# Kernel tuning notes

Measured on AMD Instinct MI355X. Metric: run time of the kernel, lower is better.

Reference implementation:

```python
import jax, jax.numpy as jnp
import numpy as np
from jax import lax

DIM = 128
HEADS = 4
HEAD_DIM = DIM // HEADS          # 32
SR = 2
BN_EPS = 1e-5


def setup_inputs() -> dict:
    key = jax.random.key(0)
    ks = jax.random.split(key, 16)
    B, N, C = 8, 3136, DIM
    H = W = 56
    Nkv = (H // SR) * (W // SR)  # 784
    s = 0.05
    inp = {
        "x": jax.random.normal(ks[0], (B, N, C), jnp.float32),
        "relative_pos": jax.random.normal(ks[1], (HEADS, N, Nkv), jnp.float32),
        "Wq": jax.random.normal(ks[2], (C, C), jnp.float32) * s,
        "bq": jnp.zeros((C,), jnp.float32),
        "Wk": jax.random.normal(ks[3], (C, C), jnp.float32) * s,
        "bk": jnp.zeros((C,), jnp.float32),
        "Wv": jax.random.normal(ks[4], (C, C), jnp.float32) * s,
        "bv": jnp.zeros((C,), jnp.float32),
        "conv_w": jax.random.normal(ks[5], (C, 1, SR, SR), jnp.float32) * s,  # depthwise OIHW
        "conv_b": jnp.zeros((C,), jnp.float32),
        "bn_gamma": jnp.ones((C,), jnp.float32),
        "bn_beta": jnp.zeros((C,), jnp.float32),
        "bn_mean": jax.random.normal(ks[6], (C,), jnp.float32) * 0.1,
        "bn_var": jax.random.uniform(ks[7], (C,), jnp.float32, 0.5, 1.5),
        "Wp": jax.random.normal(ks[8], (C, C), jnp.float32) * s,
        "bp": jnp.zeros((C,), jnp.float32),
        "H": H,
        "W": W,
    }
    return inp


def reference(x, relative_pos, Wq, bq, Wk, bk, Wv, bv, conv_w, conv_b,
              bn_gamma, bn_beta, bn_mean, bn_var, Wp, bp, H, W):
    B, N, C = x.shape
    scale = HEAD_DIM ** -0.5

    # q: (B, heads, N, head_dim)
    q = (x @ Wq + bq).reshape(B, N, HEADS, HEAD_DIM).transpose(0, 2, 1, 3)

    # spatial reduction: depthwise conv stride SR + BatchNorm (eval, running stats)
    x_img = x.transpose(0, 2, 1).reshape(B, C, H, W)
    y = lax.conv_general_dilated(
        x_img, conv_w, window_strides=(SR, SR), padding="VALID",
        feature_group_count=C,
        dimension_numbers=("NCHW", "OIHW", "NCHW")) + conv_b[None, :, None, None]
    inv = bn_gamma * lax.rsqrt(bn_var + BN_EPS)
    y = y * inv[None, :, None, None] + (bn_beta - bn_mean * inv)[None, :, None, None]
    x_ = y.reshape(B, C, -1).transpose(0, 2, 1)  # (B, Nkv, C)
    Nkv = x_.shape[1]

    k = (x_ @ Wk + bk).reshape(B, Nkv, HEADS, HEAD_DIM).transpose(0, 2, 1, 3)
    v = (x_ @ Wv + bv).reshape(B, Nkv, HEADS, HEAD_DIM).transpose(0, 2, 1, 3)

    attn = jnp.einsum("bhnd,bhmd->bhnm", q, k) * scale + relative_pos[None]
    attn = jax.nn.softmax(attn, axis=-1)
    out = jnp.einsum("bhnm,bhmd->bhnd", attn, v)
    out = out.transpose(0, 2, 1, 3).reshape(B, N, C)
    return out @ Wp + bp
```

## Files before the change

kernel.cpp:

```cpp
#include <hip/hip_runtime.h>
#include <hip/hip_bf16.h>

#define BATCH 8
#define NQ 3136
#define CDIM 128
#define NHEAD 4
#define HD 32
#define NKV 784
#define HIMG 56
#define SCALE 0.17677669529663687f

typedef __attribute__((ext_vector_type(8))) short bf8_t;
typedef __attribute__((ext_vector_type(4))) float f4_t;

using bf16 = __hip_bfloat16;
using u16  = unsigned short;

static __device__ __forceinline__ float b2f(bf16 v){ return __bfloat162float(v); }
static __device__ __forceinline__ bf16  f2b(float v){ return __float2bfloat16(v); }
static __device__ __forceinline__ short f2s(float v){
  union { bf16 b; short s; } u; u.b = f2b(v); return u.s;
}
static __device__ __forceinline__ float ld1(const void* p, size_t i, int f){
  return f ? b2f(((const bf16*)p)[i]) : ((const float*)p)[i];
}
static __device__ __forceinline__ bf8_t ld8(const void* p, size_t i, int f){
  if (f) return *(const bf8_t*)((const bf16*)p + i);
  const float* fp = (const float*)p + i;
  float4 a = *(const float4*)fp;
  float4 b = *(const float4*)(fp + 4);
  bf8_t r;
  r[0]=f2s(a.x); r[1]=f2s(a.y); r[2]=f2s(a.z); r[3]=f2s(a.w);
  r[4]=f2s(b.x); r[5]=f2s(b.y); r[6]=f2s(b.z); r[7]=f2s(b.w);
  return r;
}
static __device__ __forceinline__ int detect_flag(const void* var_raw){
  const u16* h = (const u16*)var_raw;
  int lane = threadIdx.x & 63;
  bool ok = true;
  #pragma unroll
  for (int t = 0; t < 2; t++){
    union { u16 u; bf16 b; } cv; cv.u = h[lane + 64*t];
    float v = b2f(cv.b);
    ok = ok && (v > 0.3f) && (v < 1.7f);
  }
  return (__ballot(ok) == ~0ull) ? 1 : 0;
}

static __device__ __forceinline__ void mfma_row(
    const bf8_t a[4], const bf16* __restrict__ Wt, int m, int g, f4_t acc[8])
{
  #pragma unroll
  for (int ct = 0; ct < 8; ct++){
    f4_t c = {0.f,0.f,0.f,0.f};
    const bf16* bp = Wt + (size_t)(ct*16 + m)*CDIM + 8*g;
    #pragma unroll
    for (int ks = 0; ks < 4; ks++){
      bf8_t b = *(const bf8_t*)(bp + 32*ks);
      c = __builtin_amdgcn_mfma_f32_16x16x32_bf16(a[ks], b, c, 0,0,0);
    }
    acc[ct] = c;
  }
}

__global__ __launch_bounds__(256) void prep_kernel(
    const void* __restrict__ Wq, const void* __restrict__ Wk,
    const void* __restrict__ Wv, const void* __restrict__ Wp,
    const void* __restrict__ var, const void* __restrict__ cw,
    const void* __restrict__ cb, const void* __restrict__ gam,
    const void* __restrict__ bet, const void* __restrict__ mea,
    const void* __restrict__ bq, const void* __restrict__ bk,
    const void* __restrict__ bv, const void* __restrict__ bp,
    bf16* __restrict__ Wqt, bf16* __restrict__ Wkt,
    bf16* __restrict__ Wvt, bf16* __restrict__ Wpt,
    bf16* __restrict__ bqs, bf16* __restrict__ bks,
    bf16* __restrict__ bvs, bf16* __restrict__ bps,
    float* __restrict__ cwf, float* __restrict__ inv, float* __restrict__ shift2)
{
  int f = detect_flag(var);
  int idx = blockIdx.x*256 + threadIdx.x;
  int mat = idx >> 14;
  int e   = idx & 16383;
  int o = e >> 7, i = e & 127;
  const void* src; bf16* dst; float s = 1.f;
  if      (mat == 0){ src = Wq; dst = Wqt; s = SCALE; }
  else if (mat == 1){ src = Wk; dst = Wkt; }
  else if (mat == 2){ src = Wv; dst = Wvt; }
  else              { src = Wp; dst = Wpt; }
  dst[e] = f2b(ld1(src, (size_t)i*128 + o, f) * s);

  if (blockIdx.x == 0){
    int t = threadIdx.x;
    cwf[t]       = ld1(cw, t, f);
    cwf[t + 256] = ld1(cw, t + 256, f);
    if (t < 128){
      bqs[t] = f2b(ld1(bq, t, f) * SCALE);
      bks[t] = f2b(ld1(bk, t, f));
      bvs[t] = f2b(ld1(bv, t, f));
      bps[t] = f2b(ld1(bp, t, f));
      float iv = ld1(gam, t, f) * rsqrtf(ld1(var, t, f) + 1e-5f);
      inv[t] = iv;
      shift2[t] = ld1(bet, t, f) - ld1(mea, t, f) * iv + ld1(cb, t, f) * iv;
    }
  }
}

__global__ __launch_bounds__(256) void fat_kernel(
    const void* __restrict__ x, const void* __restrict__ var,
    const float* __restrict__ cwf, const float* __restrict__ inv,
    const float* __restrict__ shift2, bf16* __restrict__ xr,
    const bf16* __restrict__ Wqt, const bf16* __restrict__ bqs,
    bf16* __restrict__ qbf)
{
  int f = detect_flag(var);
  if (blockIdx.x < 3136){
    int idx = blockIdx.x*256 + threadIdx.x;
    int c  = idx & 127;
    int t  = idx >> 7;
    int b  = t / NKV;
    int kv = t - b*NKV;
    int i = kv/28, j = kv - i*28;
    size_t base = (size_t)(b*NQ + 2*i*HIMG + 2*j)*CDIM + c;
    float acc = ld1(x, base, f)                   * cwf[c*4 + 0]
              + ld1(x, base + CDIM, f)            * cwf[c*4 + 1]
              + ld1(x, base + HIMG*CDIM, f)       * cwf[c*4 + 2]
              + ld1(x, base + HIMG*CDIM + CDIM, f)* cwf[c*4 + 3];
    xr[idx] = f2b(acc * inv[c] + shift2[c]);
  } else {
    int wave = threadIdx.x >> 6, lane = threadIdx.x & 63;
    int m = lane & 15, g = lane >> 4;
    int task = (blockIdx.x - 3136)*4 + wave;
    int row0 = task*16;
    bf8_t a[4];
    #pragma unroll
    for (int ks = 0; ks < 4; ks++)
      a[ks] = ld8(x, (size_t)(row0 + m)*CDIM + 8*g + 32*ks, f);
    f4_t acc[8];
    mfma_row(a, Wqt, m, g, acc);
    #pragma unroll
    for (int ct = 0; ct < 8; ct++){
      int col = ct*16 + m;
      float bv = b2f(bqs[col]);
      #pragma unroll
      for (int r = 0; r < 4; r++)
        qbf[(size_t)(row0 + 4*g + r)*CDIM + col] = f2b(acc[ct][r] + bv);
    }
  }
}

__global__ __launch_bounds__(256) void kv_kernel(
    const bf16* __restrict__ xr,
    const bf16* __restrict__ Wkt, const bf16* __restrict__ Wvt,
    const bf16* __restrict__ bks, const bf16* __restrict__ bvs,
    bf16* __restrict__ kbf, bf16* __restrict__ vtb)
{
  int wave = threadIdx.x >> 6, lane = threadIdx.x & 63;
  int m = lane & 15, g = lane >> 4;
  bool isK = blockIdx.x < 98;
  int bx = isK ? blockIdx.x : blockIdx.x - 98;
  int row0 = (bx*4 + wave)*16;
  bf8_t a[4];
  #pragma unroll
  for (int ks = 0; ks < 4; ks++)
    a[ks] = *(const bf8_t*)(xr + (size_t)(row0 + m)*CDIM + 8*g + 32*ks);
  f4_t acc[8];
  mfma_row(a, isK ? Wkt : Wvt, m, g, acc);

  if (isK){
    #pragma unroll
    for (int ct = 0; ct < 8; ct++){
      int col = ct*16 + m;
      float bv = b2f(bks[col]);
      #pragma unroll
      for (int r = 0; r < 4; r++)
        kbf[(size_t)(row0 + 4*g + r)*CDIM + col] = f2b(acc[ct][r] + bv);
    }
  } else {
    int b   = row0 / NKV;
    int kv0 = row0 - b*NKV + 4*g;
    #pragma unroll
    for (int ct = 0; ct < 8; ct++){
      int col = ct*16 + m;
      float bv = b2f(bvs[col]);
      int h = col >> 5, d = col & 31;
      union { bf16 hh[4]; uint2 u; } pk;
      #pragma unroll
      for (int r = 0; r < 4; r++) pk.hh[r] = f2b(acc[ct][r] + bv);
      *(uint2*)(vtb + (size_t)((b*NHEAD + h)*HD + d)*NKV + kv0) = pk.u;
    }
  }
}

template<int W>
static __device__ __forceinline__ void stage_rel(
    const void* __restrict__ rel, int f, bf16* __restrict__ rel_l,
    size_t rowbase, int kv0)
{
  const int tid = threadIdx.x;
  if (f){
    constexpr int PER = W/8;
    constexpr int SL  = 64*PER;
    #pragma unroll
    for (int it = 0; it < (SL + 255)/256; it++){
      int s0 = it*256 + tid;
      if (SL < 256 && s0 >= SL) continue;
      int row = s0 / PER;
      int col = (s0 - row*PER)*8;
      const bf16* gp = (const bf16*)rel + (rowbase + row)*NKV + kv0 + col;
      uint2 lo = *(const uint2*)gp;
      uint2 hi = *(const uint2*)(gp + 4);
      *(uint2*)(rel_l + row*132 + col)     = lo;
      *(uint2*)(rel_l + row*132 + col + 4) = hi;
    }
  } else {
    constexpr int PER = W/4;
    constexpr int SL  = 64*PER;
    #pragma unroll
    for (int it = 0; it < (SL + 255)/256; it++){
      int s0 = it*256 + tid;
      int row = s0 / PER;
      int col = (s0 - row*PER)*4;
      const float* gp = (const float*)rel + (rowbase + row)*NKV + kv0 + col;
      float4 v = *(const float4*)gp;
      union { u16 hh[4]; uint2 u; } pk;
      pk.hh[0]=(u16)f2s(v.x); pk.hh[1]=(u16)f2s(v.y);
      pk.hh[2]=(u16)f2s(v.z); pk.hh[3]=(u16)f2s(v.w);
      *(uint2*)(rel_l + row*132 + col) = pk.u;
    }
  }
}

template<int T>
static __device__ __forceinline__ void attn_chunk(
    int kv0, const bf16* __restrict__ kbase,
    const bf16* __restrict__ vb0, const bf16* __restrict__ vb1,
    const bf16* __restrict__ rel_l, int wrow, bf16* pl, int m, int g,
    bf8_t q8, float m_run[4], float l_run[4], f4_t& O0, f4_t& O1)
{
  f4_t s[T];
  #pragma unroll
  for (int t = 0; t < T; t++){
    bf8_t k8 = *(const bf8_t*)(kbase + (size_t)(kv0 + t*16)*CDIM);
    f4_t z = {0.f,0.f,0.f,0.f};
    s[t] = __builtin_amdgcn_mfma_f32_16x16x32_bf16(q8, k8, z, 0,0,0);
  }
  #pragma unroll
  for (int t = 0; t < T; t++){
    #pragma unroll
    for (int r = 0; r < 4; r++)
      s[t][r] += b2f(rel_l[(wrow + 4*g + r)*132 + t*16 + m]);
  }
  float mloc[4];
  #pragma unroll
  for (int r = 0; r < 4; r++){
    float v = s[0][r];
    #pragma unroll
    for (int t = 1; t < T; t++) v = fmaxf(v, s[t][r]);
    mloc[r] = v;
  }
  #pragma unroll
  for (int xm = 1; xm < 16; xm <<= 1){
    #pragma unroll
    for (int r = 0; r < 4; r++)
      mloc[r] = fmaxf(mloc[r], __shfl_xor(mloc[r], xm, 64));
  }
  #pragma unroll
  for (int r = 0; r < 4; r++){
    float mn = fmaxf(m_run[r], mloc[r]);
    float al = __expf(m_run[r] - mn);
    m_run[r] = mn;
    l_run[r] *= al;
    O0[r] *= al; O1[r] *= al;
  }
  #pragma unroll
  for (int t = 0; t < T; t++){
    #pragma unroll
    for (int r = 0; r < 4; r++){
      float p = __expf(s[t][r] - m_run[r]);
      l_run[r] += p;
      pl[(4*g + r)*136 + t*16 + m] = f2b(p);
    }
  }
  __syncthreads();
  constexpr int NKS = (T + 1)/2;
  #pragma unroll
  for (int ks = 0; ks < NKS; ks++){
    bf8_t a8 = *(const bf8_t*)(pl + m*136 + ks*32 + 8*g);
    bf8_t v0, v1;
    if (T == 1 && g >= 2){
      bf8_t z8 = {0,0,0,0,0,0,0,0};
      a8 = z8; v0 = z8; v1 = z8;
    } else {
      v0 = *(const bf8_t*)(vb0 + kv0 + ks*32 + 8*g);
      v1 = *(const bf8_t*)(vb1 + kv0 + ks*32 + 8*g);
    }
    O0 = __builtin_amdgcn_mfma_f32_16x16x32_bf16(a8, v0, O0, 0,0,0);
    O1 = __builtin_amdgcn_mfma_f32_16x16x32_bf16(a8, v1, O1, 0,0,0);
  }
}

template<int QF>
__global__ __launch_bounds__(256) void attn_kernel(
    const bf16* __restrict__ qbf, const void* __restrict__ x,
    const bf16* __restrict__ Wqt, const bf16* __restrict__ bqs,
    const bf16* __restrict__ kb, const bf16* __restrict__ vtb,
    const void* __restrict__ rel, const void* __restrict__ var,
    void* __restrict__ dout, bf16* __restrict__ obf)
{
  int f = detect_flag(var);
  int wave = threadIdx.x >> 6, lane = threadIdx.x & 63;
  int m = lane & 15, g = lane >> 4;
  int b = blockIdx.z, h = blockIdx.y, qt = blockIdx.x;
  int qrow0 = qt*64 + wave*16;
  int wrow  = wave*16;

  __shared__ bf16 rel_l[64*132];
  __shared__ bf16 Plds[4][16*136];
  bf16* pl = Plds[wave];

  bf8_t q8;
  if constexpr (QF == 0){
    q8 = *(const bf8_t*)(qbf + (size_t)(b*NQ + qrow0 + m)*CDIM + h*HD + 8*g);
  } else {
    bf8_t xa[4];
    #pragma unroll
    for (int ks = 0; ks < 4; ks++)
      xa[ks] = ld8(x, (size_t)(b*NQ + qrow0 + m)*CDIM + 8*g + 32*ks, f);
    f4_t qc0 = {0.f,0.f,0.f,0.f}, qc1 = {0.f,0.f,0.f,0.f};
    const bf16* wp0 = Wqt + (size_t)(h*HD + m)*CDIM + 8*g;
    const bf16* wp1 = Wqt + (size_t)(h*HD + 16 + m)*CDIM + 8*g;
    #pragma unroll
    for (int ks = 0; ks < 4; ks++){
      bf8_t w0 = *(const bf8_t*)(wp0 + 32*ks);
      bf8_t w1 = *(const bf8_t*)(wp1 + 32*ks);
      qc0 = __builtin_amdgcn_mfma_f32_16x16x32_bf16(xa[ks], w0, qc0, 0,0,0);
      qc1 = __builtin_amdgcn_mfma_f32_16x16x32_bf16(xa[ks], w1, qc1, 0,0,0);
    }
    float bv0 = b2f(bqs[h*HD + m]);
    float bv1 = b2f(bqs[h*HD + 16 + m]);
    #pragma unroll
    for (int r = 0; r < 4; r++){
      pl[(4*g + r)*136 + m]      = f2b(qc0[r] + bv0);
      pl[(4*g + r)*136 + 16 + m] = f2b(qc1[r] + bv1);
    }
    q8 = *(const bf8_t*)(pl + m*136 + 8*g);
  }

  const bf16* kbase = kb  + (size_t)(b*NKV + m)*CDIM + h*HD + 8*g;
  const bf16* vb0   = vtb + (size_t)((b*NHEAD + h)*HD + m)*NKV;
  const bf16* vb1   = vtb + (size_t)((b*NHEAD + h)*HD + 16 + m)*NKV;
  size_t rowbase = (size_t)h*NQ + qt*64;

  float m_run[4], l_run[4];
  f4_t O0 = {0.f,0.f,0.f,0.f}, O1 = {0.f,0.f,0.f,0.f};
  #pragma unroll
  for (int r = 0; r < 4; r++){ m_run[r] = -1e30f; l_run[r] = 0.f; }

  #pragma unroll 1
  for (int kv0 = 0; kv0 < 768; kv0 += 128){
    stage_rel<128>(rel, f, rel_l, rowbase, kv0);
    __syncthreads();
    attn_chunk<8>(kv0, kbase, vb0, vb1, rel_l, wrow, pl, m, g, q8, m_run, l_run, O0, O1);
  }
  stage_rel<16>(rel, f, rel_l, rowbase, 768);
  __syncthreads();
  attn_chunk<1>(768, kbase, vb0, vb1, rel_l, wrow, pl, m, g, q8, m_run, l_run, O0, O1);

  #pragma unroll
  for (int xm = 1; xm < 16; xm <<= 1){
    #pragma unroll
    for (int r = 0; r < 4; r++)
      l_run[r] += __shfl_xor(l_run[r], xm, 64);
  }
  bf16* ob = f ? (bf16*)dout : obf;
  size_t orow = (size_t)(b*NQ + qrow0 + 4*g);
  #pragma unroll
  for (int r = 0; r < 4; r++){
    float iv = 1.0f / l_run[r];
    ob[(orow + r)*CDIM + h*HD + m]      = f2b(O0[r] * iv);
    ob[(orow + r)*CDIM + h*HD + 16 + m] = f2b(O1[r] * iv);
  }
}

__global__ __launch_bounds__(256) void proj_kernel(
    const bf16* A0, const bf16* A1, const bf16* __restrict__ Wt,
    const bf16* __restrict__ bias, void* outp, const void* __restrict__ var)
{
  int f = detect_flag(var);
  const bf16* A = f ? A0 : A1;
  int wave = threadIdx.x >> 6, lane = threadIdx.x & 63;
  int m = lane & 15, g = lane >> 4;
  int row0 = (blockIdx.x*4 + wave)*16;
  bf8_t a[4];
  #pragma unroll
  for (int ks = 0; ks < 4; ks++)
    a[ks] = *(const bf8_t*)(A + (size_t)(row0 + m)*CDIM + 8*g + 32*ks);
  f4_t acc[8];
  mfma_row(a, Wt, m, g, acc);
  #pragma unroll
  for (int ct = 0; ct < 8; ct++){
    int col = ct*16 + m;
    float bv = b2f(bias[col]);
    #pragma unroll
    for (int r = 0; r < 4; r++){
      size_t oi = (size_t)(row0 + 4*g + r)*CDIM + col;
      float v = acc[ct][r] + bv;
      if (f) ((bf16*)outp)[oi]  = f2b(v);
      else   ((float*)outp)[oi] = v;
    }
  }
}

extern "C" void kernel_launch(void* const* d_in, const int* in_sizes, int n_in,
                              void* d_out, int out_size, void* d_ws, size_t ws_size,
                              hipStream_t stream)
{
  const void* x   = d_in[0];
  const void* rel = d_in[1];
  const void* Wq  = d_in[2];
  const void* bq  = d_in[3];
  const void* Wk  = d_in[4];
  const void* bk  = d_in[5];
  const void* Wv  = d_in[6];
  const void* bv  = d_in[7];
  const void* cw  = d_in[8];
  const void* cb  = d_in[9];
  const void* gam = d_in[10];
  const void* bet = d_in[11];
  const void* mea = d_in[12];
  const void* var = d_in[13];
  const void* Wp  = d_in[14];
  const void* bp  = d_in[15];

  char* w = (char*)d_ws;
  auto alloc = [&](size_t bytes){
    char* p = w; w += (bytes + 255) & ~(size_t)255; return p;
  };
  bf16* Wqt = (bf16*)alloc(128*128*sizeof(bf16));
  bf16* Wkt = (bf16*)alloc(128*128*sizeof(bf16));
  bf16* Wvt = (bf16*)alloc(128*128*sizeof(bf16));
  bf16* Wpt = (bf16*)alloc(128*128*sizeof(bf16));
  bf16* bqs = (bf16*)alloc(128*sizeof(bf16));
  bf16* bks = (bf16*)alloc(128*sizeof(bf16));
  bf16* bvs = (bf16*)alloc(128*sizeof(bf16));
  bf16* bps = (bf16*)alloc(128*sizeof(bf16));
  float* cwf    = (float*)alloc(512*sizeof(float));
  float* inv    = (float*)alloc(128*sizeof(float));
  float* shift2 = (float*)alloc(128*sizeof(float));
  bf16* xr  = (bf16*)alloc((size_t)BATCH*NKV*CDIM*sizeof(bf16));
  bf16* kbf = (bf16*)alloc((size_t)BATCH*NKV*CDIM*sizeof(bf16));
  bf16* vtb = (bf16*)alloc((size_t)BATCH*NKV*CDIM*sizeof(bf16));
  bf16* obf = (bf16*)alloc((size_t)BATCH*NQ*CDIM*sizeof(bf16));

  size_t qbf_bytes = (size_t)BATCH*NQ*CDIM*sizeof(bf16);
  bool use_q = (size_t)(((char*)d_ws + ws_size) - w) >= qbf_bytes + 256;
  bf16* qbf = use_q ? (bf16*)alloc(qbf_bytes) : nullptr;

  prep_kernel<<<256, 256, 0, stream>>>(Wq, Wk, Wv, Wp, var, cw, cb, gam, bet, mea,
                                       bq, bk, bv, bp,
                                       Wqt, Wkt, Wvt, Wpt, bqs, bks, bvs, bps,
                                       cwf, inv, shift2);
  fat_kernel<<<3136 + (use_q ? 392 : 0), 256, 0, stream>>>(
      x, var, cwf, inv, shift2, xr, Wqt, bqs, qbf);
  kv_kernel<<<196, 256, 0, stream>>>(xr, Wkt, Wvt, bks, bvs, kbf, vtb);
  if (use_q)
    attn_kernel<0><<<dim3(49, NHEAD, BATCH), 256, 0, stream>>>(
        qbf, x, Wqt, bqs, kbf, vtb, rel, var, d_out, obf);
  else
    attn_kernel<1><<<dim3(49, NHEAD, BATCH), 256, 0, stream>>>(
        qbf, x, Wqt, bqs, kbf, vtb, rel, var, d_out, obf);
  proj_kernel<<<392, 256, 0, stream>>>((const bf16*)d_out, obf, Wpt, bps, d_out, var);
}
```

Before: 246.9 us.

## Pre-convert relative_pos to bf16 in MFMA fragment order inside fat kernel

Adds a stage to the fat kernel that converts relative_pos from fp32 to bf16. It writes the result into a workspace buffer laid out in the MFMA accumulator fragment order, so each lane can load its four bias values with one 8-byte read. The attention kernel then reads the bias straight from global memory instead of staging it through shared memory, which removes the per-chunk LDS staging and one __syncthreads. In exchange it adds a separate pass that reads the full fp32 relative_pos and writes it back, plus a large workspace allocation that is used only when the workspace has room for it.

```diff
diff --git a/kernel.cpp b/kernel.cpp
--- a/kernel.cpp
+++ b/kernel.cpp
@@ -9,6 +9,8 @@
 #define NKV 784
 #define HIMG 56
 #define SCALE 0.17677669529663687f
+#define NQT16 196
+#define NCT16 49
 
 typedef __attribute__((ext_vector_type(8))) short bf8_t;
 typedef __attribute__((ext_vector_type(4))) float f4_t;
@@ -20,6 +22,9 @@
 static __device__ __forceinline__ bf16  f2b(float v){ return __float2bfloat16(v); }
 static __device__ __forceinline__ short f2s(float v){
   union { bf16 b; short s; } u; u.b = f2b(v); return u.s;
+}
+static __device__ __forceinline__ float s2f(u16 s){
+  union { unsigned u; float f; } v; v.u = ((unsigned)s) << 16; return v.f;
 }
 static __device__ __forceinline__ float ld1(const void* p, size_t i, int f){
   return f ? b2f(((const bf16*)p)[i]) : ((const float*)p)[i];
@@ -110,7 +115,8 @@
     const float* __restrict__ cwf, const float* __restrict__ inv,
     const float* __restrict__ shift2, bf16* __restrict__ xr,
     const bf16* __restrict__ Wqt, const bf16* __restrict__ bqs,
-    bf16* __restrict__ qbf)
+    bf16* __restrict__ qbf, const void* __restrict__ rel,
+    bf16* __restrict__ relb, int qrel_split)
 {
   int f = detect_flag(var);
   if (blockIdx.x < 3136){
@@ -126,7 +132,7 @@
               + ld1(x, base + HIMG*CDIM, f)       * cwf[c*4 + 2]
               + ld1(x, base + HIMG*CDIM + CDIM, f)* cwf[c*4 + 3];
     xr[idx] = f2b(acc * inv[c] + shift2[c]);
-  } else {
+  } else if ((int)blockIdx.x < qrel_split){
     int wave = threadIdx.x >> 6, lane = threadIdx.x & 63;
     int m = lane & 15, g = lane >> 4;
     int task = (blockIdx.x - 3136)*4 + wave;
@@ -145,6 +151,22 @@
       for (int r = 0; r < 4; r++)
         qbf[(size_t)(row0 + 4*g + r)*CDIM + col] = f2b(acc[ct][r] + bv);
     }
+  } else {
+    int idx = (blockIdx.x - qrel_split)*256 + threadIdx.x;
+    int lane = idx & 63;
+    int rest = idx >> 6;
+    int c = rest % NCT16;
+    int ht = rest / NCT16;
+    int t = ht % NQT16;
+    int h = ht / NQT16;
+    int m = lane & 15, g = lane >> 4;
+    int row = t*16 + 4*g;
+    int col = c*16 + m;
+    union { u16 hh[4]; uint2 u; } pk;
+    #pragma unroll
+    for (int r = 0; r < 4; r++)
+      pk.hh[r] = (u16)f2s(ld1(rel, ((size_t)h*NQ + row + r)*NKV + col, f));
+    *(uint2*)(relb + (size_t)idx*4) = pk.u;
   }
 }
 
@@ -230,11 +252,12 @@
   }
 }
 
-template<int T>
+template<int T, int RB>
 static __device__ __forceinline__ void attn_chunk(
     int kv0, const bf16* __restrict__ kbase,
     const bf16* __restrict__ vb0, const bf16* __restrict__ vb1,
-    const bf16* __restrict__ rel_l, int wrow, bf16* pl, int m, int g,
+    const bf16* __restrict__ relt, const bf16* __restrict__ rel_l, int wrow,
+    bf16* pl, int m, int g, int lane,
     bf8_t q8, float m_run[4], float l_run[4], f4_t& O0, f4_t& O1)
 {
   f4_t s[T];
@@ -244,11 +267,22 @@
     f4_t z = {0.f,0.f,0.f,0.f};
     s[t] = __builtin_amdgcn_mfma_f32_16x16x32_bf16(q8, k8, z, 0,0,0);
   }
-  #pragma unroll
-  for (int t = 0; t < T; t++){
-    #pragma unroll
-    for (int r = 0; r < 4; r++)
-      s[t][r] += b2f(rel_l[(wrow + 4*g + r)*132 + t*16 + m]);
+  if (RB){
+    int c0 = kv0 >> 4;
+    #pragma unroll
+    for (int t = 0; t < T; t++){
+      union { uint2 u; u16 hh[4]; } rl;
+      rl.u = *(const uint2*)(relt + (size_t)((c0 + t)*64 + lane)*4);
+      #pragma unroll
+      for (int r = 0; r < 4; r++) s[t][r] += s2f(rl.hh[r]);
+    }
+  } else {
+    #pragma unroll
+    for (int t = 0; t < T; t++){
+      #pragma unroll
+      for (int r = 0; r < 4; r++)
+        s[t][r] += b2f(rel_l[(wrow + 4*g + r)*132 + t*16 + m]);
+    }
   }
   float mloc[4];
   #pragma unroll
@@ -281,7 +315,7 @@
       pl[(4*g + r)*136 + t*16 + m] = f2b(p);
     }
   }
-  __syncthreads();
+  if (!RB) __syncthreads();
   constexpr int NKS = (T + 1)/2;
   #pragma unroll
   for (int ks = 0; ks < NKS; ks++){
@@ -299,12 +333,13 @@
   }
 }
 
-template<int QF>
+template<int QF, int RB>
 __global__ __launch_bounds__(256) void attn_kernel(
     const bf16* __restrict__ qbf, const void* __restrict__ x,
     const bf16* __restrict__ Wqt, const bf16* __restrict__ bqs,
     const bf16* __restrict__ kb, const bf16* __restrict__ vtb,
-    const void* __restrict__ rel, const void* __restrict__ var,
+    const void* __restrict__ rel, const bf16* __restrict__ relb,
+    const void* __restrict__ var,
     void* __restrict__ dout, bf16* __restrict__ obf)
 {
   int f = detect_flag(var);
@@ -314,7 +349,7 @@
   int qrow0 = qt*64 + wave*16;
   int wrow  = wave*16;
 
-  __shared__ bf16 rel_l[64*132];
+  __shared__ bf16 rel_l[RB ? 2 : 64*132];
   __shared__ bf16 Plds[4][16*136];
   bf16* pl = Plds[wave];
 
@@ -350,6 +385,8 @@
   const bf16* vb0   = vtb + (size_t)((b*NHEAD + h)*HD + m)*NKV;
   const bf16* vb1   = vtb + (size_t)((b*NHEAD + h)*HD + 16 + m)*NKV;
   size_t rowbase = (size_t)h*NQ + qt*64;
+  const bf16* relt = relb +
+      (size_t)((h*NQT16 + (qrow0 >> 4)) * NCT16) * 64 * 4;
 
   float m_run[4], l_run[4];
   f4_t O0 = {0.f,0.f,0.f,0.f}, O1 = {0.f,0.f,0.f,0.f};
@@ -358,13 +395,19 @@
 
   #pragma unroll 1
   for (int kv0 = 0; kv0 < 768; kv0 += 128){
-    stage_rel<128>(rel, f, rel_l, rowbase, kv0);
+    if (!RB){
+      stage_rel<128>(rel, f, rel_l, rowbase, kv0);
+      __syncthreads();
+    }
+    attn_chunk<8, RB>(kv0, kbase, vb0, vb1, relt, rel_l, wrow, pl, m, g, lane,
+                      q8, m_run, l_run, O0, O1);
+  }
+  if (!RB){
+    stage_rel<16>(rel, f, rel_l, rowbase, 768);
     __syncthreads();
-    attn_chunk<8>(kv0, kbase, vb0, vb1, rel_l, wrow, pl, m, g, q8, m_run, l_run, O0, O1);
-  }
-  stage_rel<16>(rel, f, rel_l, rowbase, 768);
-  __syncthreads();
-  attn_chunk<1>(768, kbase, vb0, vb1, rel_l, wrow, pl, m, g, q8, m_run, l_run, O0, O1);
+  }
+  attn_chunk<1, RB>(768, kbase, vb0, vb1, relt, rel_l, wrow, pl, m, g, lane,
+                    q8, m_run, l_run, O0, O1);
 
   #pragma unroll
   for (int xm = 1; xm < 16; xm <<= 1){
@@ -433,6 +476,7 @@
   const void* bp  = d_in[15];
 
   char* w = (char*)d_ws;
+  char* wend = (char*)d_ws + ws_size;
   auto alloc = [&](size_t bytes){
     char* p = w; w += (bytes + 255) & ~(size_t)255; return p;
   };
@@ -452,22 +496,34 @@
   bf16* vtb = (bf16*)alloc((size_t)BATCH*NKV*CDIM*sizeof(bf16));
   bf16* obf = (bf16*)alloc((size_t)BATCH*NQ*CDIM*sizeof(bf16));
 
-  size_t qbf_bytes = (size_t)BATCH*NQ*CDIM*sizeof(bf16);
-  bool use_q = (size_t)(((char*)d_ws + ws_size) - w) >= qbf_bytes + 256;
+  size_t qbf_bytes  = (size_t)BATCH*NQ*CDIM*sizeof(bf16);
+  bool use_q = (size_t)(wend - w) >= qbf_bytes + 256;
   bf16* qbf = use_q ? (bf16*)alloc(qbf_bytes) : nullptr;
+
+  size_t relb_bytes = (size_t)NHEAD*NQ*NKV*sizeof(bf16);
+  bool use_rb = (size_t)(wend - w) >= relb_bytes + 256;
+  bf16* relb = use_rb ? (bf16*)alloc(relb_bytes) : nullptr;
+
+  int qrel_split = 3136 + (use_q ? 392 : 0);
+  int nblk = qrel_split + (use_rb ? (NHEAD*NQT16*NCT16*64*4)/1024 : 0);
 
   prep_kernel<<<256, 256, 0, stream>>>(Wq, Wk, Wv, Wp, var, cw, cb, gam, bet, mea,
                                        bq, bk, bv, bp,
                                        Wqt, Wkt, Wvt, Wpt, bqs, bks, bvs, bps,
                                        cwf, inv, shift2);
-  fat_kernel<<<3136 + (use_q ? 392 : 0), 256, 0, stream>>>(
-      x, var, cwf, inv, shift2, xr, Wqt, bqs, qbf);
+  fat_kernel<<<nblk, 256, 0, stream>>>(
+      x, var, cwf, inv, shift2, xr, Wqt, bqs, qbf, rel, relb, qrel_split);
   kv_kernel<<<196, 256, 0, stream>>>(xr, Wkt, Wvt, bks, bvs, kbf, vtb);
-  if (use_q)
-    attn_kernel<0><<<dim3(49, NHEAD, BATCH), 256, 0, stream>>>(
-        qbf, x, Wqt, bqs, kbf, vtb, rel, var, d_out, obf);
+
+  dim3 ag(49, NHEAD, BATCH);
+  if (use_q && use_rb)
+    attn_kernel<0,1><<<ag, 256, 0, stream>>>(qbf, x, Wqt, bqs, kbf, vtb, rel, relb, var, d_out, obf);
+  else if (use_q)
+    attn_kernel<0,0><<<ag, 256, 0, stream>>>(qbf, x, Wqt, bqs, kbf, vtb, rel, relb, var, d_out, obf);
+  else if (use_rb)
+    attn_kernel<1,1><<<ag, 256, 0, stream>>>(qbf, x, Wqt, bqs, kbf, vtb, rel, relb, var, d_out, obf);
   else
-    attn_kernel<1><<<dim3(49, NHEAD, BATCH), 256, 0, stream>>>(
-        qbf, x, Wqt, bqs, kbf, vtb, rel, var, d_out, obf);
+    attn_kernel<1,0><<<ag, 256, 0, stream>>>(qbf, x, Wqt, bqs, kbf, vtb, rel, relb, var, d_out, obf);
+
   proj_kernel<<<392, 256, 0, stream>>>((const bf16*)d_out, obf, Wpt, bps, d_out, var);
 }
```

New measurement: 263.0 us. 1.07x slower.

## Pre-swizzle relative_pos into MFMA layout and drop online-softmax max tracking

Applied to the files above, without the earlier changes.

A new rel_kernel converts relative_pos once per call into bf16, pre-scaled by log2(e) and laid out in MFMA accumulator-tile order. The kv axis is padded to 896, with large-negative bias entries and zeroed K/V rows. The attention loop then feeds the bias straight in as the MFMA accumulator, uses exp2, prefetches the next chunk of K and bias in registers, and drops the shared-memory staging, __syncthreads and running-max rescaling. This removes the repeated fp32 rel reads across batches and the per-chunk barrier and max reductions. In exchange it adds an extra pass over rel and relies on the scores staying small enough that an unshifted exp2 does not overflow.

```diff
diff --git a/kernel.cpp b/kernel.cpp
--- a/kernel.cpp
+++ b/kernel.cpp
@@ -7,8 +7,12 @@
 #define NHEAD 4
 #define HD 32
 #define NKV 784
+#define NKVP 896
 #define HIMG 56
 #define SCALE 0.17677669529663687f
+#define L2E 1.44269504f
+#define NQT16 196
+#define NCT 56
 
 typedef __attribute__((ext_vector_type(8))) short bf8_t;
 typedef __attribute__((ext_vector_type(4))) float f4_t;
@@ -83,7 +87,7 @@
   int e   = idx & 16383;
   int o = e >> 7, i = e & 127;
   const void* src; bf16* dst; float s = 1.f;
-  if      (mat == 0){ src = Wq; dst = Wqt; s = SCALE; }
+  if      (mat == 0){ src = Wq; dst = Wqt; s = SCALE * L2E; }
   else if (mat == 1){ src = Wk; dst = Wkt; }
   else if (mat == 2){ src = Wv; dst = Wvt; }
   else              { src = Wp; dst = Wpt; }
@@ -94,7 +98,7 @@
     cwf[t]       = ld1(cw, t, f);
     cwf[t + 256] = ld1(cw, t + 256, f);
     if (t < 128){
-      bqs[t] = f2b(ld1(bq, t, f) * SCALE);
+      bqs[t] = f2b(ld1(bq, t, f) * SCALE * L2E);
       bks[t] = f2b(ld1(bk, t, f));
       bvs[t] = f2b(ld1(bv, t, f));
       bps[t] = f2b(ld1(bp, t, f));
@@ -148,12 +152,81 @@
   }
 }
 
+__global__ __launch_bounds__(256) void rel_kernel(
+    const void* __restrict__ rel, const void* __restrict__ var,
+    bf16* __restrict__ relb)
+{
+  int f = detect_flag(var);
+  int h   = blockIdx.x / NQT16;
+  int t16 = blockIdx.x - h*NQT16;
+  int tid = threadIdx.x;
+  __shared__ u16 srel[16*NKVP];
+
+  if (f){
+    for (int u = tid; u < 16*98; u += 256){
+      int row = u / 98, c8 = u - row*98;
+      const bf16* gp = (const bf16*)rel + ((size_t)h*NQ + t16*16 + row)*NKV + c8*8;
+      union { uint4 q; u16 hh[8]; } in; in.q = *(const uint4*)gp;
+      u16* dp = srel + row*NKVP + c8*8;
+      #pragma unroll
+      for (int e = 0; e < 8; e++){
+        union { unsigned u; float ff; } cv; cv.u = ((unsigned)in.hh[e]) << 16;
+        dp[e] = (u16)f2s(cv.ff * L2E);
+      }
+    }
+  } else {
+    for (int u = tid; u < 16*196; u += 256){
+      int row = u / 196, c4 = u - row*196;
+      const float* gp = (const float*)rel + ((size_t)h*NQ + t16*16 + row)*NKV + c4*4;
+      float4 v = *(const float4*)gp;
+      u16* dp = srel + row*NKVP + c4*4;
+      dp[0] = (u16)f2s(v.x*L2E); dp[1] = (u16)f2s(v.y*L2E);
+      dp[2] = (u16)f2s(v.z*L2E); dp[3] = (u16)f2s(v.w*L2E);
+    }
+  }
+  for (int u = tid; u < 16*28; u += 256){
+    int row = u / 28, c4 = u - row*28;
+    *(uint2*)(srel + row*NKVP + 784 + c4*4) = make_uint2(0xFF7FFF7Fu, 0xFF7FFF7Fu);
+  }
+  __syncthreads();
+
+  bf16* outb = relb + (size_t)(h*NQT16 + t16)*NCT*256;
+  for (int u = tid; u < NCT*64; u += 256){
+    int tile = u >> 6, ln = u & 63;
+    int mm = ln & 15, gg = ln >> 4;
+    const u16* sp = srel + (4*gg)*NKVP + tile*16 + mm;
+    union { u16 hh[4]; uint2 q; } pk;
+    #pragma unroll
+    for (int r = 0; r < 4; r++) pk.hh[r] = sp[r*NKVP];
+    *(uint2*)(outb + (size_t)u*4) = pk.q;
+  }
+}
+
 __global__ __launch_bounds__(256) void kv_kernel(
     const bf16* __restrict__ xr,
     const bf16* __restrict__ Wkt, const bf16* __restrict__ Wvt,
     const bf16* __restrict__ bks, const bf16* __restrict__ bvs,
-    bf16* __restrict__ kbf, bf16* __restrict__ vtb)
-{
+    bf16* __restrict__ kbf2, bf16* __restrict__ vtb2)
+{
+  if (blockIdx.x >= 196){
+    int u0 = (blockIdx.x - 196)*256 + threadIdx.x;
+    #pragma unroll
+    for (int j = 0; j < 4; j++){
+      int u = u0*4 + j;
+      bf16* p;
+      if (u < 14336){
+        int b = u / 1792, r = u - b*1792;
+        int row = r >> 4, cu = r & 15;
+        p = kbf2 + (size_t)(b*NKVP + 784 + row)*CDIM + cu*8;
+      } else {
+        int v = u - 14336;
+        int row = v / 14, cu = v - row*14;
+        p = vtb2 + (size_t)row*NKVP + 784 + cu*8;
+      }
+      *(uint4*)p = make_uint4(0,0,0,0);
+    }
+    return;
+  }
   int wave = threadIdx.x >> 6, lane = threadIdx.x & 63;
   int m = lane & 15, g = lane >> 4;
   bool isK = blockIdx.x < 98;
@@ -166,6 +239,8 @@
   f4_t acc[8];
   mfma_row(a, isK ? Wkt : Wvt, m, g, acc);
 
+  int b   = row0 / NKV;
+  int kvr = row0 - b*NKV;
   if (isK){
     #pragma unroll
     for (int ct = 0; ct < 8; ct++){
@@ -173,11 +248,10 @@
       float bv = b2f(bks[col]);
       #pragma unroll
       for (int r = 0; r < 4; r++)
-        kbf[(size_t)(row0 + 4*g + r)*CDIM + col] = f2b(acc[ct][r] + bv);
+        kbf2[(size_t)(b*NKVP + kvr + 4*g + r)*CDIM + col] = f2b(acc[ct][r] + bv);
     }
   } else {
-    int b   = row0 / NKV;
-    int kv0 = row0 - b*NKV + 4*g;
+    int kv0 = kvr + 4*g;
     #pragma unroll
     for (int ct = 0; ct < 8; ct++){
       int col = ct*16 + m;
@@ -186,116 +260,8 @@
       union { bf16 hh[4]; uint2 u; } pk;
       #pragma unroll
       for (int r = 0; r < 4; r++) pk.hh[r] = f2b(acc[ct][r] + bv);
-      *(uint2*)(vtb + (size_t)((b*NHEAD + h)*HD + d)*NKV + kv0) = pk.u;
-    }
-  }
-}
-
-template<int W>
-static __device__ __forceinline__ void stage_rel(
-    const void* __restrict__ rel, int f, bf16* __restrict__ rel_l,
-    size_t rowbase, int kv0)
-{
-  const int tid = threadIdx.x;
-  if (f){
-    constexpr int PER = W/8;
-    constexpr int SL  = 64*PER;
-    #pragma unroll
-    for (int it = 0; it < (SL + 255)/256; it++){
-      int s0 = it*256 + tid;
-      if (SL < 256 && s0 >= SL) continue;
-      int row = s0 / PER;
-      int col = (s0 - row*PER)*8;
-      const bf16* gp = (const bf16*)rel + (rowbase + row)*NKV + kv0 + col;
-      uint2 lo = *(const uint2*)gp;
-      uint2 hi = *(const uint2*)(gp + 4);
-      *(uint2*)(rel_l + row*132 + col)     = lo;
-      *(uint2*)(rel_l + row*132 + col + 4) = hi;
-    }
-  } else {
-    constexpr int PER = W/4;
-    constexpr int SL  = 64*PER;
-    #pragma unroll
-    for (int it = 0; it < (SL + 255)/256; it++){
-      int s0 = it*256 + tid;
-      int row = s0 / PER;
-      int col = (s0 - row*PER)*4;
-      const float* gp = (const float*)rel + (rowbase + row)*NKV + kv0 + col;
-      float4 v = *(const float4*)gp;
-      union { u16 hh[4]; uint2 u; } pk;
-      pk.hh[0]=(u16)f2s(v.x); pk.hh[1]=(u16)f2s(v.y);
-      pk.hh[2]=(u16)f2s(v.z); pk.hh[3]=(u16)f2s(v.w);
-      *(uint2*)(rel_l + row*132 + col) = pk.u;
-    }
-  }
-}
-
-template<int T>
-static __device__ __forceinline__ void attn_chunk(
-    int kv0, const bf16* __restrict__ kbase,
-    const bf16* __restrict__ vb0, const bf16* __restrict__ vb1,
-    const bf16* __restrict__ rel_l, int wrow, bf16* pl, int m, int g,
-    bf8_t q8, float m_run[4], float l_run[4], f4_t& O0, f4_t& O1)
-{
-  f4_t s[T];
-  #pragma unroll
-  for (int t = 0; t < T; t++){
-    bf8_t k8 = *(const bf8_t*)(kbase + (size_t)(kv0 + t*16)*CDIM);
-    f4_t z = {0.f,0.f,0.f,0.f};
-    s[t] = __builtin_amdgcn_mfma_f32_16x16x32_bf16(q8, k8, z, 0,0,0);
-  }
-  #pragma unroll
-  for (int t = 0; t < T; t++){
-    #pragma unroll
-    for (int r = 0; r < 4; r++)
-      s[t][r] += b2f(rel_l[(wrow + 4*g + r)*132 + t*16 + m]);
-  }
-  float mloc[4];
-  #pragma unroll
-  for (int r = 0; r < 4; r++){
-    float v = s[0][r];
-    #pragma unroll
-    for (int t = 1; t < T; t++) v = fmaxf(v, s[t][r]);
-    mloc[r] = v;
-  }
-  #pragma unroll
-  for (int xm = 1; xm < 16; xm <<= 1){
-    #pragma unroll
-    for (int r = 0; r < 4; r++)
-      mloc[r] = fmaxf(mloc[r], __shfl_xor(mloc[r], xm, 64));
-  }
-  #pragma unroll
-  for (int r = 0; r < 4; r++){
-    float mn = fmaxf(m_run[r], mloc[r]);
-    float al = __expf(m_run[r] - mn);
-    m_run[r] = mn;
-    l_run[r] *= al;
-    O0[r] *= al; O1[r] *= al;
-  }
-  #pragma unroll
-  for (int t = 0; t < T; t++){
-    #pragma unroll
-    for (int r = 0; r < 4; r++){
-      float p = __expf(s[t][r] - m_run[r]);
-      l_run[r] += p;
-      pl[(4*g + r)*136 + t*16 + m] = f2b(p);
-    }
-  }
-  __syncthreads();
-  constexpr int NKS = (T + 1)/2;
-  #pragma unroll
-  for (int ks = 0; ks < NKS; ks++){
-    bf8_t a8 = *(const bf8_t*)(pl + m*136 + ks*32 + 8*g);
-    bf8_t v0, v1;
-    if (T == 1 && g >= 2){
-      bf8_t z8 = {0,0,0,0,0,0,0,0};
-      a8 = z8; v0 = z8; v1 = z8;
-    } else {
-      v0 = *(const bf8_t*)(vb0 + kv0 + ks*32 + 8*g);
-      v1 = *(const bf8_t*)(vb1 + kv0 + ks*32 + 8*g);
-    }
-    O0 = __builtin_amdgcn_mfma_f32_16x16x32_bf16(a8, v0, O0, 0,0,0);
-    O1 = __builtin_amdgcn_mfma_f32_16x16x32_bf16(a8, v1, O1, 0,0,0);
+      *(uint2*)(vtb2 + (size_t)((b*NHEAD + h)*HD + d)*NKVP + kv0) = pk.u;
+    }
   }
 }
 
@@ -303,8 +269,8 @@
 __global__ __launch_bounds__(256) void attn_kernel(
     const bf16* __restrict__ qbf, const void* __restrict__ x,
     const bf16* __restrict__ Wqt, const bf16* __restrict__ bqs,
-    const bf16* __restrict__ kb, const bf16* __restrict__ vtb,
-    const void* __restrict__ rel, const void* __restrict__ var,
+    const bf16* __restrict__ kb2, const bf16* __restrict__ vtb2,
+    const bf16* __restrict__ relb, const void* __restrict__ var,
     void* __restrict__ dout, bf16* __restrict__ obf)
 {
   int f = detect_flag(var);
@@ -312,9 +278,7 @@
   int m = lane & 15, g = lane >> 4;
   int b = blockIdx.z, h = blockIdx.y, qt = blockIdx.x;
   int qrow0 = qt*64 + wave*16;
-  int wrow  = wave*16;
-
-  __shared__ bf16 rel_l[64*132];
+
   __shared__ bf16 Plds[4][16*136];
   bf16* pl = Plds[wave];
 
@@ -346,25 +310,57 @@
     q8 = *(const bf8_t*)(pl + m*136 + 8*g);
   }
 
-  const bf16* kbase = kb  + (size_t)(b*NKV + m)*CDIM + h*HD + 8*g;
-  const bf16* vb0   = vtb + (size_t)((b*NHEAD + h)*HD + m)*NKV;
-  const bf16* vb1   = vtb + (size_t)((b*NHEAD + h)*HD + 16 + m)*NKV;
-  size_t rowbase = (size_t)h*NQ + qt*64;
-
-  float m_run[4], l_run[4];
+  const bf16* kbase = kb2 + (size_t)(b*NKVP + m)*CDIM + h*HD + 8*g;
+  const bf16* vb0   = vtb2 + (size_t)((b*NHEAD + h)*HD + m)*NKVP;
+  const bf16* vb1   = vb0 + (size_t)16*NKVP;
+  const bf16* relt  = relb + (size_t)(h*NQT16 + (qrow0 >> 4))*NCT*256;
+
+  float l_run[4] = {0.f,0.f,0.f,0.f};
   f4_t O0 = {0.f,0.f,0.f,0.f}, O1 = {0.f,0.f,0.f,0.f};
-  #pragma unroll
-  for (int r = 0; r < 4; r++){ m_run[r] = -1e30f; l_run[r] = 0.f; }
+
+  bf8_t kc[8]; uint2 rl[8];
+  #pragma unroll
+  for (int t = 0; t < 8; t++){
+    kc[t] = *(const bf8_t*)(kbase + (size_t)(t*16)*CDIM);
+    rl[t] = *(const uint2*)(relt + (size_t)(t*64 + lane)*4);
+  }
 
   #pragma unroll 1
-  for (int kv0 = 0; kv0 < 768; kv0 += 128){
-    stage_rel<128>(rel, f, rel_l, rowbase, kv0);
-    __syncthreads();
-    attn_chunk<8>(kv0, kbase, vb0, vb1, rel_l, wrow, pl, m, g, q8, m_run, l_run, O0, O1);
-  }
-  stage_rel<16>(rel, f, rel_l, rowbase, 768);
-  __syncthreads();
-  attn_chunk<1>(768, kbase, vb0, vb1, rel_l, wrow, pl, m, g, q8, m_run, l_run, O0, O1);
+  for (int c = 0; c < 7; c++){
+    int cn = (c < 6) ? c + 1 : 6;
+    bf8_t kn[8]; uint2 rn[8];
+    #pragma unroll
+    for (int t = 0; t < 8; t++){
+      kn[t] = *(const bf8_t*)(kbase + (size_t)(cn*128 + t*16)*CDIM);
+      rn[t] = *(const uint2*)(relt + (size_t)((cn*8 + t)*64 + lane)*4);
+    }
+    int kv0 = c*128;
+    #pragma unroll
+    for (int t = 0; t < 8; t++){
+      f4_t rc;
+      rc[0] = __uint_as_float(rl[t].x << 16);
+      rc[1] = __uint_as_float(rl[t].x & 0xffff0000u);
+      rc[2] = __uint_as_float(rl[t].y << 16);
+      rc[3] = __uint_as_float(rl[t].y & 0xffff0000u);
+      f4_t s = __builtin_amdgcn_mfma_f32_16x16x32_bf16(q8, kc[t], rc, 0,0,0);
+      #pragma unroll
+      for (int r = 0; r < 4; r++){
+        float p = exp2f(s[r]);
+        l_run[r] += p;
+        pl[(4*g + r)*136 + t*16 + m] = f2b(p);
+      }
+    }
+    #pragma unroll
+    for (int ks = 0; ks < 4; ks++){
+      bf8_t a8 = *(const bf8_t*)(pl + m*136 + ks*32 + 8*g);
+      bf8_t v0 = *(const bf8_t*)(vb0 + kv0 + ks*32 + 8*g);
+      bf8_t v1 = *(const bf8_t*)(vb1 + kv0 + ks*32 + 8*g);
+      O0 = __builtin_amdgcn_mfma_f32_16x16x32_bf16(a8, v0, O0, 0,0,0);
+      O1 = __builtin_amdgcn_mfma_f32_16x16x32_bf16(a8, v1, O1, 0,0,0);
+    }
+    #pragma unroll
+    for (int t = 0; t < 8; t++){ kc[t] = kn[t]; rl[t] = rn[t]; }
+  }
 
   #pragma unroll
   for (int xm = 1; xm < 16; xm <<= 1){
@@ -433,6 +429,7 @@
   const void* bp  = d_in[15];
 
   char* w = (char*)d_ws;
+  char* wend = (char*)d_ws + ws_size;
   auto alloc = [&](size_t bytes){
     char* p = w; w += (bytes + 255) & ~(size_t)255; return p;
   };
@@ -447,13 +444,13 @@
   float* cwf    = (float*)alloc(512*sizeof(float));
   float* inv    = (float*)alloc(128*sizeof(float));
   float* shift2 = (float*)alloc(128*sizeof(float));
-  bf16* xr  = (bf16*)alloc((size_t)BATCH*NKV*CDIM*sizeof(bf16));
-  bf16* kbf = (bf16*)alloc((size_t)BATCH*NKV*CDIM*sizeof(bf16));
-  bf16* vtb = (bf16*)alloc((size_t)BATCH*NKV*CDIM*sizeof(bf16));
-  bf16* obf = (bf16*)alloc((size_t)BATCH*NQ*CDIM*sizeof(bf16));
-
+  bf16* xr   = (bf16*)alloc((size_t)BATCH*NKV*CDIM*sizeof(bf16));
+  bf16* kbf2 = (bf16*)alloc((size_t)BATCH*NKVP*CDIM*sizeof(bf16));
+  bf16* vtb2 = (bf16*)alloc((size_t)BATCH*NHEAD*HD*NKVP*sizeof(bf16));
+  bf16* obf  = (bf16*)alloc((size_t)BATCH*NQ*CDIM*sizeof(bf16));
+  bf16* relb = (bf16*)alloc((size_t)NHEAD*NQT16*NCT*256*sizeof(bf16));
   size_t qbf_bytes = (size_t)BATCH*NQ*CDIM*sizeof(bf16);
-  bool use_q = (size_t)(((char*)d_ws + ws_size) - w) >= qbf_bytes + 256;
+  bool use_q = (size_t)(wend - w) >= qbf_bytes + 256;
   bf16* qbf = use_q ? (bf16*)alloc(qbf_bytes) : nullptr;
 
   prep_kernel<<<256, 256, 0, stream>>>(Wq, Wk, Wv, Wp, var, cw, cb, gam, bet, mea,
@@ -462,12 +459,14 @@
                                        cwf, inv, shift2);
   fat_kernel<<<3136 + (use_q ? 392 : 0), 256, 0, stream>>>(
       x, var, cwf, inv, shift2, xr, Wqt, bqs, qbf);
-  kv_kernel<<<196, 256, 0, stream>>>(xr, Wkt, Wvt, bks, bvs, kbf, vtb);
+  rel_kernel<<<NHEAD*NQT16, 256, 0, stream>>>(rel, var, relb);
+  kv_kernel<<<224, 256, 0, stream>>>(xr, Wkt, Wvt, bks, bvs, kbf2, vtb2);
+
+  dim3 ag(49, NHEAD, BATCH);
   if (use_q)
-    attn_kernel<0><<<dim3(49, NHEAD, BATCH), 256, 0, stream>>>(
-        qbf, x, Wqt, bqs, kbf, vtb, rel, var, d_out, obf);
+    attn_kernel<0><<<ag, 256, 0, stream>>>(qbf, x, Wqt, bqs, kbf2, vtb2, relb, var, d_out, obf);
   else
-    attn_kernel<1><<<dim3(49, NHEAD, BATCH), 256, 0, stream>>>(
-        qbf, x, Wqt, bqs, kbf, vtb, rel, var, d_out, obf);
+    attn_kernel<1><<<ag, 256, 0, stream>>>(qbf, x, Wqt, bqs, kbf2, vtb2, relb, var, d_out, obf);
+
   proj_kernel<<<392, 256, 0, stream>>>((const bf16*)d_out, obf, Wpt, bps, d_out, var);
 }
```

Result: slower. 284.2 us (+15.1%).
